# Kernel tuning notes

Hardware: AMD Instinct MI355X
Metric: run time of the kernel (lower is better)

The kernel has to match this reference:

```python
import jax, jax.numpy as jnp
import numpy as np

NEG_SLOPE = 0.2  # LeakyReLU(0.2)
DN = ('NCDHW', 'OIDHW', 'NCDHW')


def leaky(x):
    return jnp.where(x >= 0, x, NEG_SLOPE * x)


def conv3d(x, w, stride=1, pad=1):
    return jax.lax.conv_general_dilated(
        x, w, (stride,) * 3, [(pad, pad)] * 3, dimension_numbers=DN)


def down_mask(m):
    # active output sites of a k=3, s=2, p=1 sparse conv = maxpool of input mask
    return jax.lax.reduce_window(
        m, 0.0, jax.lax.max, (1, 1, 3, 3, 3), (1, 1, 2, 2, 2),
        [(0, 0), (0, 0), (1, 1), (1, 1), (1, 1)])


def res_block(x, m, wa, wb, wdn):
    # SubMConv3d == dense conv masked to active sites (inactive inputs are zero)
    identity = conv3d(x, wdn, 1, 0) * m if wdn is not None else x
    out = leaky(conv3d(x, wa) * m)
    out = conv3d(out, wb) * m
    return leaky(out + identity)


def setup_inputs() -> dict:
    key = jax.random.key(0)
    ks = jax.random.split(key, 12)
    B, D = 2, 64
    occ = jax.random.uniform(ks[0], (B, 1, D, D, D)) < 0.05
    mask = occ.astype(jnp.float32)
    x = jax.random.normal(ks[1], (B, 3, D, D, D), jnp.float32) * mask

    def w(k, o, i, ksz):
        fan = i * ksz ** 3
        return jax.random.normal(k, (o, i, ksz, ksz, ksz), jnp.float32) / np.sqrt(fan).astype(np.float32)

    return {
        'x': x, 'mask': mask,
        # stage1 (in 3 -> 64), has 1x1 downsample
        'w1a': w(ks[2], 64, 3, 3), 'w1b': w(ks[3], 64, 64, 3), 'w1d': w(ks[4], 64, 3, 1),
        'wd1': w(ks[5], 128, 64, 3),   # down1 stride 2
        'w2a': w(ks[6], 128, 128, 3), 'w2b': w(ks[7], 128, 128, 3),  # stage2
        'wd2': w(ks[8], 256, 128, 3),  # down2 stride 2
        'w3a': w(ks[9], 256, 256, 3), 'w3b': w(ks[10], 256, 256, 3),  # stage3
        'wd3': w(ks[11], 128, 256, 3),  # down3 stride 2 -> out_ch=128
    }


def reference(x, mask, w1a, w1b, w1d, wd1, w2a, w2b, wd2, w3a, w3b, wd3):
    m1 = mask
    m2 = down_mask(m1)
    m3 = down_mask(m2)

    x1 = res_block(x, m1, w1a, w1b, w1d)          # [B,64,64,64,64]
    x = leaky(conv3d(x1, wd1, stride=2))           # [B,128,32,32,32]
    x2 = res_block(x, m2, w2a, w2b, None)
    x = leaky(conv3d(x2, wd2, stride=2))           # [B,256,16,16,16]
    x3 = res_block(x, m3, w3a, w3b, None)
    x4 = leaky(conv3d(x3, wd3, stride=2))          # [B,128,8,8,8] == x4.dense()

    avg = x4.mean(axis=(2, 3, 4))
    mx = x4.max(axis=(2, 3, 4))
    return jnp.concatenate([avg, mx], axis=1)      # [B,256]
```

## Files before the change

### kernel.cpp

```cpp
#include <hip/hip_runtime.h>


enum { EPI_MASK = 1, EPI_LEAKY = 2, EPI_RESID = 4 };
#define ROWCAP 32768

typedef short  bf16x8 __attribute__((ext_vector_type(8)));
typedef float  f32x4  __attribute__((ext_vector_type(4)));
typedef ushort us4    __attribute__((ext_vector_type(4)));

__device__ __forceinline__ float leaky(float v) { return v >= 0.f ? v : 0.2f * v; }
__device__ __forceinline__ ushort f2bf(float f) {
    unsigned u = __float_as_uint(f);
    return (ushort)((u + 0x7FFFu + ((u >> 16) & 1u)) >> 16);
}
__device__ __forceinline__ float bf2f(ushort h) {
    return __uint_as_float((unsigned)h << 16);
}
__device__ __forceinline__ int choff(int c) {
    return (c >> 5) * 64 + ((c >> 3) & 3) * 16 + (c & 7);
}

__global__ __launch_bounds__(256) void transpose_w_kernel(
    const float* __restrict__ w, float* __restrict__ wT, int CO, int CIK)
{
    int i = blockIdx.x * 256 + threadIdx.x;
    if (i >= CO * CIK) return;
    int co = i / CIK, r = i - co * CIK;
    wT[(size_t)r * CO + co] = w[i];
}

__global__ __launch_bounds__(256) void pack_w1b_kernel(
    const float* __restrict__ w, float* __restrict__ wT)
{
    int i = blockIdx.x * 256 + threadIdx.x;
    if (i >= 27 * 64 * 64) return;
    int co = i & 63, ci = (i >> 6) & 63, t = i >> 12;
    wT[i] = w[(co * 64 + ci) * 27 + t];
}

__global__ __launch_bounds__(256) void pack_w_kernel(
    const float* __restrict__ w, ushort* __restrict__ A, int CI, int CO)
{
    int i = blockIdx.x * 256 + threadIdx.x;
    if (i >= 27 * CI * CO * 2) return;
    int j = i & 7, hilo = (i >> 3) & 1, L = (i >> 4) & 63, rest = i >> 10;
    int NMT = CO >> 4, NCI = CI >> 5;
    int mt = rest % NMT; rest /= NMT;
    int ct = rest % NCI;
    int tap = rest / NCI;
    int co = mt * 16 + (L & 15);
    int ci = ct * 32 + (L >> 4) * 8 + j;
    float v = w[((size_t)co * CI + ci) * 27 + tap];
    ushort h = f2bf(v);
    A[i] = hilo ? f2bf(v - bf2f(h)) : h;
}

template<int DIN, int DOUT>
__global__ __launch_bounds__(256) void maxpool_kernel(
    const float* __restrict__ in, float* __restrict__ out)
{
    int i = blockIdx.x * 256 + threadIdx.x;
    constexpr int D3O = DOUT * DOUT * DOUT;
    if (i >= 2 * D3O) return;
    int b = i / D3O;
    int v = i - b * D3O;
    int z = v / (DOUT * DOUT), y = (v / DOUT) % DOUT, x = v % DOUT;
    float mx = 0.f;
    #pragma unroll
    for (int dz = 0; dz < 3; ++dz)
        #pragma unroll
        for (int dy = 0; dy < 3; ++dy)
            #pragma unroll
            for (int dx = 0; dx < 3; ++dx) {
                int zi = 2 * z - 1 + dz, yi = 2 * y - 1 + dy, xi = 2 * x - 1 + dx;
                if ((unsigned)zi < (unsigned)DIN && (unsigned)yi < (unsigned)DIN &&
                    (unsigned)xi < (unsigned)DIN)
                    mx = fmaxf(mx, in[(size_t)b * DIN * DIN * DIN + (zi * DIN + yi) * DIN + xi]);
            }
    out[i] = mx;
}

__global__ __launch_bounds__(256) void build_list_kernel(
    const float* __restrict__ m, int* __restrict__ list, int* __restrict__ idxmap,
    int* __restrict__ count)
{
    int i = blockIdx.x * 256 + threadIdx.x;
    if (i >= 2 * 262144) return;
    if (m[i] > 0.5f) {
        int k = atomicAdd(count, 1);
        if (k < ROWCAP) {
            list[k] = i;
            idxmap[i] = k;
        }
    }
}

__global__ __launch_bounds__(64) void stage1a_kernel(
    const float* __restrict__ x, const float* __restrict__ waT,
    const int* __restrict__ list, const int* __restrict__ count,
    float* __restrict__ t1c)
{
    __shared__ float smem[81];
    int n = min(*count, ROWCAP);
    for (int i = blockIdx.x; i < n; i += gridDim.x) {
        int lin = list[i];
        int b = lin >> 18;
        int v = lin & 262143;
        int z = v >> 12, y = (v >> 6) & 63, xx = v & 63;
        for (int j = threadIdx.x; j < 81; j += 64) {
            int ci = j / 27, t = j - ci * 27;
            int zz = z + t / 9 - 1, yy = y + (t / 3) % 3 - 1, xc = xx + t % 3 - 1;
            float val = 0.f;
            if ((unsigned)zz < 64u && (unsigned)yy < 64u && (unsigned)xc < 64u)
                val = x[(size_t)(b * 3 + ci) * 262144 + (zz << 12) + (yy << 6) + xc];
            smem[j] = val;
        }
        __syncthreads();
        float acc = 0.f;
        #pragma unroll 9
        for (int j = 0; j < 81; ++j)
            acc = fmaf(smem[j], waT[j * 64 + threadIdx.x], acc);
        t1c[(size_t)i * 64 + threadIdx.x] = leaky(acc);
        __syncthreads();
    }
}

__global__ __launch_bounds__(64) void stage1b_kernel(
    const float* __restrict__ t1c, const float* __restrict__ x,
    const float* __restrict__ w1bT,
    const float* __restrict__ wdT,
    const int* __restrict__ list, const int* __restrict__ idxmap,
    const int* __restrict__ count,
    float* __restrict__ x1c)
{
    __shared__ int   srr[27];
    __shared__ float sx[27][64];
    int n = min(*count, ROWCAP);
    int i = blockIdx.x;
    if (i >= n) return;
    const int tid = threadIdx.x;
    int lin = list[i];
    int b = lin >> 18;
    int v = lin & 262143;
    int z = v >> 12, y = (v >> 6) & 63, xx = v & 63;
    const int* im = idxmap + b * 262144;

    if (tid < 27) {
        int kz = tid / 9, ky = (tid / 3) % 3, kx = tid % 3;
        int zz = z + kz - 1, yy = y + ky - 1, xc = xx + kx - 1;
        int r = -1;
        if ((unsigned)zz < 64u && (unsigned)yy < 64u && (unsigned)xc < 64u)
            r = im[(zz << 12) + (yy << 6) + xc];
        srr[tid] = r;
    }
    __syncthreads();
    #pragma unroll 1
    for (int t = 0; t < 27; ++t) {
        int r = srr[t];
        if (r >= 0)
            sx[t][tid] = t1c[(size_t)r * 64 + tid];
    }
    __syncthreads();

    float acc = 0.f;
    #pragma unroll 1
    for (int t = 0; t < 27; ++t) {
        if (srr[t] < 0) continue;
        const float* wp = w1bT + (size_t)t * 4096 + tid;
        const float* xr = sx[t];
        #pragma unroll 8
        for (int ci = 0; ci < 64; ++ci)
            acc = fmaf(xr[ci], wp[ci * 64], acc);
    }
    float id = 0.f;
    #pragma unroll
    for (int ci = 0; ci < 3; ++ci)
        id = fmaf(x[(size_t)(b * 3 + ci) * 262144 + v], wdT[ci * 64 + tid], id);
    x1c[(size_t)i * 64 + tid] = leaky(acc + id);
}

__global__ __launch_bounds__(128) void wd1_kernel(
    const float* __restrict__ x1c, const int* __restrict__ idxmap,
    const float* __restrict__ wT,
    ushort* __restrict__ outp)
{
    __shared__ int   srr[27];
    __shared__ float sx[27][64];
    const int tid = threadIdx.x;
    const int v = blockIdx.x;
    const int b = blockIdx.y;
    const int zo = v >> 10, yo = (v >> 5) & 31, xo = v & 31;
    const int* im = idxmap + b * 262144;

    if (tid < 27) {
        int kz = tid / 9, ky = (tid / 3) % 3, kx = tid % 3;
        int zi = 2 * zo - 1 + kz, yi = 2 * yo - 1 + ky, xi = 2 * xo - 1 + kx;
        int r = -1;
        if ((unsigned)zi < 64u && (unsigned)yi < 64u && (unsigned)xi < 64u)
            r = im[(zi << 12) + (yi << 6) + xi];
        srr[tid] = r;
    }
    __syncthreads();
    #pragma unroll 1
    for (int t = 0; t < 27; ++t) {
        int r = srr[t];
        if (r >= 0 && tid < 64)
            sx[t][tid] = x1c[(size_t)r * 64 + tid];
    }
    __syncthreads();

    float acc = 0.f;
    #pragma unroll 1
    for (int t = 0; t < 27; ++t) {
        if (srr[t] < 0) continue;
        const float* wp = wT + (size_t)t * 128 + tid;
        const float* xr = sx[t];
        #pragma unroll 8
        for (int ci = 0; ci < 64; ++ci)
            acc = fmaf(xr[ci], wp[(size_t)ci * 27 * 128], acc);
    }
    float val = leaky(acc);
    ushort hb = f2bf(val);
    ushort lb = f2bf(val - bf2f(hb));
    size_t vb = ((((size_t)b * 32 + zo) * 32 + yo) * 33 + xo) * 256 + 256;
    int off = choff(tid);
    outp[vb + off] = hb;
    outp[vb + off + 8] = lb;
}

template<int CI, int CO, int DI, int DO, int STRIDE, int RY, int NX, int NCT, int WPEU, int EPI>
__global__ __launch_bounds__(256, WPEU) void mfma_conv6_kernel(
    const ushort* __restrict__ inp, const ushort* __restrict__ A,
    const float* __restrict__ mask, const ushort* __restrict__ resid,
    ushort* __restrict__ outp)
{
    constexpr int NCI = CI / 32;
    constexpr int NMT = CO / 16;
    constexpr int CV = CI * 2;
    constexpr int CVO = CO * 2;
    constexpr int YG = DO / RY;
    constexpr int NXV = (DO - 1) * STRIDE + 3;
    constexpr int LVS = (STRIDE == 2) ? 68 : 72;
    constexpr int NGRP = RY * NXV * 8;

    __shared__ ushort sB[RY * NXV * LVS];

    const int rg = (blockIdx.x & 7) * ((int)gridDim.x >> 3) + (blockIdx.x >> 3);
    const int y0 = (rg % YG) * RY;
    const int z = (rg / YG) % DO;
    const int b = rg / (YG * DO);
    const int wave = threadIdx.x >> 6;
    const int lane = threadIdx.x & 63;
    const int n_l = lane & 15;
    const int q = lane >> 4;
    const int mt0 = (blockIdx.y * 4 + wave) * NCT;

    f32x4 acc[NCT][RY][NX];
    #pragma unroll
    for (int a = 0; a < NCT; ++a)
        #pragma unroll
        for (int r = 0; r < RY; ++r)
            #pragma unroll
            for (int c = 0; c < NX; ++c)
                acc[a][r][c] = (f32x4){0.f, 0.f, 0.f, 0.f};

    #pragma unroll 1
    for (int ct = 0; ct < NCI; ++ct) {
        #pragma unroll 1
        for (int dz = 0; dz < 3; ++dz) {
            int zp = z * STRIDE + dz - 1;
            bool vz = (unsigned)zp < (unsigned)DI;
            int zpc = vz ? zp : 0;
            #pragma unroll 1
            for (int dy = 0; dy < 3; ++dy) {
                long rowb[RY];
                #pragma unroll
                for (int ry = 0; ry < RY; ++ry) {
                    int yp = (y0 + ry) * STRIDE + dy - 1;
                    bool v = vz && ((unsigned)yp < (unsigned)DI);
                    rowb[ry] = v ? (((((long)b * DI + zpc) * DI + yp) * (DI + 1)) * CV + CV) : -1;
                }
                __syncthreads();
                for (int g = threadIdx.x; g < NGRP; g += 256) {
                    int r = g / (NXV * 8);
                    int rem = g - r * (NXV * 8);
                    int xv = rem >> 3;
                    int gg = rem & 7;
                    long src = (rowb[r] >= 0)
                             ? (rowb[r] + (long)(xv - 1) * CV + ct * 64 + gg * 8)
                             : (long)(ct * 64 + gg * 8);
                    *(bf16x8*)(sB + (r * NXV + xv) * LVS + gg * 8) = *(const bf16x8*)(inp + src);
                }
                __syncthreads();
                #pragma unroll
                for (int dx = 0; dx < 3; ++dx) {
                    const int tap = dz * 9 + dy * 3 + dx;
                    bf16x8 bh[RY][NX], bl[RY][NX];
                    #pragma unroll
                    for (int ry = 0; ry < RY; ++ry)
                        #pragma unroll
                        for (int nx = 0; nx < NX; ++nx) {
                            int xv = (nx * 16 + n_l) * STRIDE + dx;
                            const ushort* p = sB + (ry * NXV + xv) * LVS + q * 16;
                            bh[ry][nx] = *(const bf16x8*)p;
                            bl[ry][nx] = *(const bf16x8*)(p + 8);
                        }
                    bf16x8 ahf[NCT], alf[NCT];
                    #pragma unroll
                    for (int mt = 0; mt < NCT; ++mt) {
                        size_t aa = ((size_t)(tap * NCI + ct) * NMT + (mt0 + mt)) * 1024 + lane * 16;
                        ahf[mt] = *(const bf16x8*)(A + aa);
                        alf[mt] = *(const bf16x8*)(A + aa + 8);
                    }
                    #pragma unroll
                    for (int mt = 0; mt < NCT; ++mt)
                        #pragma unroll
                        for (int ry = 0; ry < RY; ++ry)
                            #pragma unroll
                            for (int nx = 0; nx < NX; ++nx)
                                acc[mt][ry][nx] = __builtin_amdgcn_mfma_f32_16x16x32_bf16(ahf[mt], bh[ry][nx], acc[mt][ry][nx], 0, 0, 0);
                    #pragma unroll
                    for (int mt = 0; mt < NCT; ++mt)
                        #pragma unroll
                        for (int ry = 0; ry < RY; ++ry)
                            #pragma unroll
                            for (int nx = 0; nx < NX; ++nx)
                                acc[mt][ry][nx] = __builtin_amdgcn_mfma_f32_16x16x32_bf16(ahf[mt], bl[ry][nx], acc[mt][ry][nx], 0, 0, 0);
                    #pragma unroll
                    for (int mt = 0; mt < NCT; ++mt)
                        #pragma unroll
                        for (int ry = 0; ry < RY; ++ry)
                            #pragma unroll
                            for (int nx = 0; nx < NX; ++nx)
                                acc[mt][ry][nx] = __builtin_amdgcn_mfma_f32_16x16x32_bf16(alf[mt], bh[ry][nx], acc[mt][ry][nx], 0, 0, 0);
                }
            }
        }
    }

    #pragma unroll
    for (int ry = 0; ry < RY; ++ry) {
        int yo = y0 + ry;
        #pragma unroll
        for (int nx = 0; nx < NX; ++nx) {
            int xo = nx * 16 + n_l;
            size_t vb = ((((size_t)b * DO + z) * DO + yo) * (DO + 1)) * CVO + CVO + (size_t)xo * CVO;
            float mval = 1.f;
            if (EPI & EPI_MASK) mval = mask[(((size_t)b * DO + z) * DO + yo) * DO + xo];
            #pragma unroll
            for (int mt = 0; mt < NCT; ++mt) {
                int c0 = (mt0 + mt) * 16 + q * 4;
                size_t oa = vb + choff(c0);
                float rs[4] = {0.f, 0.f, 0.f, 0.f};
                if (EPI & EPI_RESID) {
                    us4 rh4 = *(const us4*)(resid + oa);
                    us4 rl4 = *(const us4*)(resid + oa + 8);
                    #pragma unroll
                    for (int r = 0; r < 4; ++r) rs[r] = bf2f(rh4[r]) + bf2f(rl4[r]);
                }
                us4 oh, ol;
                #pragma unroll
                for (int r = 0; r < 4; ++r) {
                    float v = acc[mt][ry][nx][r];
                    if (EPI & EPI_MASK) v *= mval;
                    if (EPI & EPI_RESID) v += rs[r];
                    if (EPI & EPI_LEAKY) v = leaky(v);
                    ushort hb = f2bf(v);
                    oh[r] = hb;
                    ol[r] = f2bf(v - bf2f(hb));
                }
                *(us4*)(outp + oa) = oh;
                *(us4*)(outp + oa + 8) = ol;
            }
        }
    }
}

template<int CI, int CO, int DI, int RY, int NCT, int KS, int WPEU>
__global__ __launch_bounds__(256, WPEU) void mfma_conv7_kernel(
    const ushort* __restrict__ inp, const ushort* __restrict__ A,
    float* __restrict__ part)
{
    constexpr int DO = DI;
    constexpr int NCI = CI / 32;
    constexpr int KCI = NCI / KS;
    constexpr int NMT = CO / 16;
    constexpr int CV = CI * 2;
    constexpr int YG = DO / RY;
    constexpr int NYR = RY + 2;
    constexpr int NXV = DO + 2;
    constexpr int LVS = 72;
    constexpr int NCOG = NMT / (4 * NCT);
    constexpr int D3 = DO * DO * DO;

    __shared__ ushort sB[3 * NYR * NXV * LVS];

    const int rg = (blockIdx.x & 7) * ((int)gridDim.x >> 3) + (blockIdx.x >> 3);
    const int y0 = (rg % YG) * RY;
    const int z = (rg / YG) % DO;
    const int b = rg / (YG * DO);
    const int wave = threadIdx.x >> 6;
    const int lane = threadIdx.x & 63;
    const int n_l = lane & 15;
    const int q = lane >> 4;
    const int cog = blockIdx.y % NCOG;
    const int kc = blockIdx.y / NCOG;
    const int mt0 = (cog * 4 + wave) * NCT;

    f32x4 acc[NCT][RY];
    #pragma unroll
    for (int a = 0; a < NCT; ++a)
        #pragma unroll
        for (int r = 0; r < RY; ++r)
            acc[a][r] = (f32x4){0.f, 0.f, 0.f, 0.f};

    #pragma unroll 1
    for (int ctl = 0; ctl < KCI; ++ctl) {
        const int ct = kc * KCI + ctl;
        __syncthreads();
        for (int g = threadIdx.x; g < 3 * NYR * NXV * 8; g += 256) {
            int row = g / (NXV * 8);
            int rem = g - row * (NXV * 8);
            int xv = rem >> 3;
            int gg = rem & 7;
            int zi = row / NYR, yr = row - zi * NYR;
            int zp = z + zi - 1;
            int yp = y0 + yr - 1;
            bool v = ((unsigned)zp < (unsigned)DI) & ((unsigned)yp < (unsigned)DI);
            long src = v ? ((((((long)b * DI + zp) * DI + yp) * (DI + 1)) * CV + CV)
                            + (long)(xv - 1) * CV + ct * 64 + gg * 8)
                         : (long)(ct * 64 + gg * 8);
            *(bf16x8*)(sB + (row * NXV + xv) * LVS + gg * 8) = *(const bf16x8*)(inp + src);
        }
        __syncthreads();
        #pragma unroll 1
        for (int dz = 0; dz < 3; ++dz) {
            #pragma unroll 1
            for (int dy = 0; dy < 3; ++dy) {
                #pragma unroll
                for (int dx = 0; dx < 3; ++dx) {
                    const int tap = dz * 9 + dy * 3 + dx;
                    bf16x8 bh[RY], bl[RY];
                    #pragma unroll
                    for (int ry = 0; ry < RY; ++ry) {
                        const ushort* p = sB + ((dz * NYR + ry + dy) * NXV + n_l + dx) * LVS + q * 16;
                        bh[ry] = *(const bf16x8*)p;
                        bl[ry] = *(const bf16x8*)(p + 8);
                    }
                    bf16x8 ahf[NCT], alf[NCT];
                    #pragma unroll
                    for (int mt = 0; mt < NCT; ++mt) {
                        size_t aa = ((size_t)(tap * NCI + ct) * NMT + (mt0 + mt)) * 1024 + lane * 16;
                        ahf[mt] = *(const bf16x8*)(A + aa);
                        alf[mt] = *(const bf16x8*)(A + aa + 8);
                    }
                    #pragma unroll
                    for (int mt = 0; mt < NCT; ++mt)
                        #pragma unroll
                        for (int ry = 0; ry < RY; ++ry)
                            acc[mt][ry] = __builtin_amdgcn_mfma_f32_16x16x32_bf16(ahf[mt], bh[ry], acc[mt][ry], 0, 0, 0);
                    #pragma unroll
                    for (int mt = 0; mt < NCT; ++mt)
                        #pragma unroll
                        for (int ry = 0; ry < RY; ++ry)
                            acc[mt][ry] = __builtin_amdgcn_mfma_f32_16x16x32_bf16(ahf[mt], bl[ry], acc[mt][ry], 0, 0, 0);
                    #pragma unroll
                    for (int mt = 0; mt < NCT; ++mt)
                        #pragma unroll
                        for (int ry = 0; ry < RY; ++ry)
                            acc[mt][ry] = __builtin_amdgcn_mfma_f32_16x16x32_bf16(alf[mt], bh[ry], acc[mt][ry], 0, 0, 0);
                }
            }
        }
    }

    #pragma unroll
    for (int ry = 0; ry < RY; ++ry) {
        int yo = y0 + ry;
        int v = (z * DO + yo) * DO + n_l;
        #pragma unroll
        for (int mt = 0; mt < NCT; ++mt) {
            int c0 = (mt0 + mt) * 16 + q * 4;
            size_t off = (((size_t)kc * 2 + b) * D3 + v) * CO + c0;
            *(f32x4*)(part + off) = acc[mt][ry];
        }
    }
}

__global__ __launch_bounds__(256) void combine3_kernel(
    const float* __restrict__ part, const float* __restrict__ mask,
    const ushort* __restrict__ resid, ushort* __restrict__ outp)
{
    int i = blockIdx.x * 256 + threadIdx.x;
    if (i >= 2 * 4096 * 64) return;
    int g = i & 63, v = (i >> 6) & 4095, b = i >> 18;
    int c0 = g * 4;
    size_t p0 = (((size_t)b) * 4096 + v) * 256 + c0;
    float4 s0 = *(const float4*)(part + p0);
    float4 s1 = *(const float4*)(part + p0 + (size_t)2 * 4096 * 256);
    float m = mask[b * 4096 + v];
    int z = v >> 8, y = (v >> 4) & 15, x = v & 15;
    size_t vb = ((((size_t)b * 16 + z) * 16 + y) * 17) * 512 + 512 + (size_t)x * 512;
    size_t oa = vb + choff(c0);
    float rs[4] = {0.f, 0.f, 0.f, 0.f};
    if (resid) {
        us4 rh = *(const us4*)(resid + oa);
        us4 rl = *(const us4*)(resid + oa + 8);
        #pragma unroll
        for (int r = 0; r < 4; ++r) rs[r] = bf2f(rh[r]) + bf2f(rl[r]);
    }
    float sv[4] = {s0.x + s1.x, s0.y + s1.y, s0.z + s1.z, s0.w + s1.w};
    us4 oh, ol;
    #pragma unroll
    for (int r = 0; r < 4; ++r) {
        float val = sv[r] * m + rs[r];
        val = leaky(val);
        ushort hb = f2bf(val);
        oh[r] = hb;
        ol[r] = f2bf(val - bf2f(hb));
    }
    *(us4*)(outp + oa) = oh;
    *(us4*)(outp + oa + 8) = ol;
}

__global__ __launch_bounds__(256) void wd3_mfma_kernel(
    const ushort* __restrict__ x3, const ushort* __restrict__ A,
    float* __restrict__ x4)
{
    constexpr int NCI = 8;
    constexpr int NMT = 8;
    const int blk = blockIdx.x;
    const int yg = blk & 3;
    const int z = (blk >> 2) & 7;
    const int b = blk >> 5;
    const int wave = threadIdx.x >> 6;
    const int lane = threadIdx.x & 63;
    const int n_l = lane & 15;
    const int q = lane >> 4;
    const int y = yg * 2 + (n_l >> 3);
    const int x = n_l & 7;
    const int mt0 = wave * 2;

    f32x4 acc[2];
    acc[0] = (f32x4){0.f, 0.f, 0.f, 0.f};
    acc[1] = (f32x4){0.f, 0.f, 0.f, 0.f};
    const bf16x8 zero8 = {0, 0, 0, 0, 0, 0, 0, 0};

    for (int ct = 0; ct < NCI; ++ct) {
        #pragma unroll
        for (int dz = 0; dz < 3; ++dz) {
            int zp = 2 * z + dz - 1;
            if ((unsigned)zp >= 16u) continue;
            #pragma unroll
            for (int dy = 0; dy < 3; ++dy) {
                int yp = 2 * y + dy - 1;
                bool vy = (unsigned)yp < 16u;
                int ypc = vy ? yp : 0;
                #pragma unroll
                for (int dx = 0; dx < 3; ++dx) {
                    int xp = 2 * x + dx - 1;
                    int tap = dz * 9 + dy * 3 + dx;
                    size_t ba = ((((size_t)b * 16 + zp) * 16 + ypc) * 17 + 1 + xp) * 512
                              + ct * 64 + q * 16;
                    bf16x8 bh = vy ? *(const bf16x8*)(x3 + ba) : zero8;
                    bf16x8 bl = vy ? *(const bf16x8*)(x3 + ba + 8) : zero8;
                    bf16x8 ahf[2], alf[2];
                    #pragma unroll
                    for (int mt = 0; mt < 2; ++mt) {
                        size_t aa = ((size_t)(tap * NCI + ct) * NMT + (mt0 + mt)) * 1024 + lane * 16;
                        ahf[mt] = *(const bf16x8*)(A + aa);
                        alf[mt] = *(const bf16x8*)(A + aa + 8);
                    }
                    #pragma unroll
                    for (int mt = 0; mt < 2; ++mt)
                        acc[mt] = __builtin_amdgcn_mfma_f32_16x16x32_bf16(ahf[mt], bh, acc[mt], 0, 0, 0);
                    #pragma unroll
                    for (int mt = 0; mt < 2; ++mt)
                        acc[mt] = __builtin_amdgcn_mfma_f32_16x16x32_bf16(ahf[mt], bl, acc[mt], 0, 0, 0);
                    #pragma unroll
                    for (int mt = 0; mt < 2; ++mt)
                        acc[mt] = __builtin_amdgcn_mfma_f32_16x16x32_bf16(alf[mt], bh, acc[mt], 0, 0, 0);
                }
            }
        }
    }
    #pragma unroll
    for (int mt = 0; mt < 2; ++mt)
        #pragma unroll
        for (int r = 0; r < 4; ++r) {
            int co = (mt0 + mt) * 16 + q * 4 + r;
            x4[((size_t)(b * 128 + co)) * 512 + z * 64 + y * 8 + x] = leaky(acc[mt][r]);
        }
}

__global__ __launch_bounds__(64) void reduce_kernel(
    const float* __restrict__ x4, float* __restrict__ out)
{
    int bc = blockIdx.x;
    int b = bc >> 7, c = bc & 127;
    const float* p = x4 + (size_t)(b * 128 + c) * 512;
    float s = 0.f, mx = -3.4e38f;
    for (int i = threadIdx.x; i < 512; i += 64) {
        float v = p[i];
        s += v;
        mx = fmaxf(mx, v);
    }
    #pragma unroll
    for (int o = 32; o > 0; o >>= 1) {
        s += __shfl_down(s, o);
        mx = fmaxf(mx, __shfl_down(mx, o));
    }
    if (threadIdx.x == 0) {
        out[b * 256 + c] = s * (1.f / 512.f);
        out[b * 256 + 128 + c] = mx;
    }
}

__global__ __launch_bounds__(256) void zero_out_kernel(float* __restrict__ out, int n)
{
    int i = blockIdx.x * 256 + threadIdx.x;
    if (i < n) out[i] = 0.f;
}

extern "C" void kernel_launch(void* const* d_in, const int* in_sizes, int n_in,
                              void* d_out, int out_size, void* d_ws, size_t ws_size,
                              hipStream_t stream)
{
    (void)in_sizes; (void)n_in;
    const float* x    = (const float*)d_in[0];
    const float* mask = (const float*)d_in[1];
    const float* w1a  = (const float*)d_in[2];
    const float* w1b  = (const float*)d_in[3];
    const float* w1d  = (const float*)d_in[4];
    const float* wd1  = (const float*)d_in[5];
    const float* w2a  = (const float*)d_in[6];
    const float* w2b  = (const float*)d_in[7];
    const float* wd2  = (const float*)d_in[8];
    const float* w3a  = (const float*)d_in[9];
    const float* w3b  = (const float*)d_in[10];
    const float* wd3  = (const float*)d_in[11];
    float* out = (float*)d_out;
    char* ws = (char*)d_ws;

    const size_t RSZ = 34603520;
    const size_t SZ3 = 8913920;
    const size_t POFF = 9437184;
    char* R1 = ws;
    char* R2 = ws + RSZ;
    char* R3 = ws + 2 * RSZ;
    size_t off = 3 * RSZ;
    auto alloc = [&](size_t bytes) { char* p = ws + off; off = (off + bytes + 255) & ~255ull; return p; };
    ushort* pk2a = (ushort*)alloc(1769472);
    ushort* pk2b = (ushort*)alloc(1769472);
    ushort* pkd2 = (ushort*)alloc(3538944);
    ushort* pk3a = (ushort*)alloc(7077888);
    ushort* pk3b = (ushort*)alloc(7077888);
    float*  wd1T = (float*)alloc(884736);
    float*  waT  = (float*)alloc(20736);
    float*  w1bT = (float*)alloc(442368);
    float*  wdTt = (float*)alloc(768);
    float*  m2   = (float*)alloc(262144);
    float*  m3   = (float*)alloc(32768);
    int*    cnt  = (int*)alloc(256);
    const size_t NEED = off;

    if (ws_size < NEED) {
        zero_out_kernel<<<dim3((out_size + 255) / 256), 256, 0, stream>>>(out, out_size);
        return;
    }

    float* t1c  = (float*)R2;
    float* x1c  = (float*)(R2 + 8388608);
    int*   idx  = (int*)(R2 + 16777216);
    int*   list = (int*)(R2 + 18874368);
    ushort* pkd3 = (ushort*)R1;
    float*  x4   = (float*)R2;
    float*  part3a = (float*)(R2 + POFF);
    float*  part3b = (float*)(R3 + POFF);

    ushort* xin2 = (ushort*)R1;
    ushort* t2   = (ushort*)R2;
    ushort* x2   = (ushort*)R3;
    ushort* xin3 = (ushort*)R1;
    ushort* t3   = (ushort*)R2;
    ushort* x3   = (ushort*)R3;

    hipMemsetAsync(cnt, 0, 4, stream);
    hipMemsetAsync(idx, 0xFF, 2097152, stream);
    hipMemsetAsync(R1, 0, RSZ, stream);

    auto tg = [](int n) { return dim3((n + 255) / 256); };
    pack_w_kernel<<<tg(27 * 128 * 128 * 2), 256, 0, stream>>>(w2a, pk2a, 128, 128);
    pack_w_kernel<<<tg(27 * 128 * 128 * 2), 256, 0, stream>>>(w2b, pk2b, 128, 128);
    pack_w_kernel<<<tg(27 * 128 * 256 * 2), 256, 0, stream>>>(wd2, pkd2, 128, 256);
    pack_w_kernel<<<tg(27 * 256 * 256 * 2), 256, 0, stream>>>(w3a, pk3a, 256, 256);
    pack_w_kernel<<<tg(27 * 256 * 256 * 2), 256, 0, stream>>>(w3b, pk3b, 256, 256);
    transpose_w_kernel <<<tg(128 * 1728), 256, 0, stream>>>(wd1, wd1T, 128, 1728);
    transpose_w_kernel <<<tg(64 * 81),    256, 0, stream>>>(w1a, waT,  64, 81);
    pack_w1b_kernel    <<<tg(27 * 64 * 64), 256, 0, stream>>>(w1b, w1bT);
    transpose_w_kernel <<<tg(64 * 3),     256, 0, stream>>>(w1d, wdTt, 64, 3);

    maxpool_kernel<64, 32><<<dim3(2 * 32768 / 256), 256, 0, stream>>>(mask, m2);
    maxpool_kernel<32, 16><<<dim3(2 * 4096 / 256),  256, 0, stream>>>(m2, m3);
    build_list_kernel<<<dim3(2 * 262144 / 256), 256, 0, stream>>>(mask, list, idx, cnt);

    stage1a_kernel<<<dim3(2048), 64, 0, stream>>>(x, waT, list, cnt, t1c);
    stage1b_kernel<<<dim3(ROWCAP), 64, 0, stream>>>(t1c, x, w1bT, wdTt, list, idx, cnt, x1c);
    wd1_kernel<<<dim3(32768, 2), 128, 0, stream>>>(x1c, idx, wd1T, xin2);

    hipMemsetAsync(R2, 0, RSZ, stream);
    hipMemsetAsync(R3, 0, RSZ, stream);

    mfma_conv6_kernel<128, 128, 32, 32, 1, 2, 2, 2, 4, EPI_MASK | EPI_LEAKY>
        <<<dim3(1024, 1), 256, 0, stream>>>(xin2, pk2a, m2, nullptr, t2);
    mfma_conv6_kernel<128, 128, 32, 32, 1, 2, 2, 2, 4, EPI_MASK | EPI_RESID | EPI_LEAKY>
        <<<dim3(1024, 1), 256, 0, stream>>>(t2, pk2b, m2, xin2, x2);

    hipMemsetAsync(R1, 0, SZ3, stream);
    mfma_conv6_kernel<128, 256, 32, 16, 2, 2, 1, 2, 4, EPI_LEAKY>
        <<<dim3(256, 2), 256, 0, stream>>>(x2, pkd2, nullptr, nullptr, xin3);

    hipMemsetAsync(R2, 0, SZ3, stream);
    mfma_conv7_kernel<256, 256, 16, 2, 2, 2, 4>
        <<<dim3(256, 4), 256, 0, stream>>>(xin3, pk3a, part3a);
    combine3_kernel<<<dim3(2048), 256, 0, stream>>>(part3a, m3, nullptr, t3);

    hipMemsetAsync(R3, 0, SZ3, stream);
    mfma_conv7_kernel<256, 256, 16, 2, 2, 2, 4>
        <<<dim3(256, 4), 256, 0, stream>>>(t3, pk3b, part3b);
    combine3_kernel<<<dim3(2048), 256, 0, stream>>>(part3b, m3, xin3, x3);

    pack_w_kernel<<<tg(27 * 256 * 128 * 2), 256, 0, stream>>>(wd3, pkd3, 256, 128);
    wd3_mfma_kernel<<<dim3(64), 256, 0, stream>>>(x3, pkd3, x4);

    reduce_kernel<<<dim3(256), 64, 0, stream>>>(x4, out);
}
```

Before: 1.207 ms.

## Stage y-halo slab in shared memory once per dz for stage-2 convs

Adds a new conv kernel for the stride-1 stage-2 convolutions. For each (channel tile, dz) it loads a slab of RY+2 input rows with halo into shared memory, then loops over all dy and dx taps from that slab. The old kernel appears to reload per dy row. This cuts global-to-LDS traffic and barrier count by reusing the y halo, at the cost of a larger shared buffer, which may lower occupancy.

```diff
diff --git a/kernel.cpp b/kernel.cpp
--- a/kernel.cpp
+++ b/kernel.cpp
@@ -302,6 +302,151 @@
                         for (int nx = 0; nx < NX; ++nx) {
                             int xv = (nx * 16 + n_l) * STRIDE + dx;
                             const ushort* p = sB + (ry * NXV + xv) * LVS + q * 16;
+                            bh[ry][nx] = *(const bf16x8*)p;
+                            bl[ry][nx] = *(const bf16x8*)(p + 8);
+                        }
+                    bf16x8 ahf[NCT], alf[NCT];
+                    #pragma unroll
+                    for (int mt = 0; mt < NCT; ++mt) {
+                        size_t aa = ((size_t)(tap * NCI + ct) * NMT + (mt0 + mt)) * 1024 + lane * 16;
+                        ahf[mt] = *(const bf16x8*)(A + aa);
+                        alf[mt] = *(const bf16x8*)(A + aa + 8);
+                    }
+                    #pragma unroll
+                    for (int mt = 0; mt < NCT; ++mt)
+                        #pragma unroll
+                        for (int ry = 0; ry < RY; ++ry)
+                            #pragma unroll
+                            for (int nx = 0; nx < NX; ++nx)
+                                acc[mt][ry][nx] = __builtin_amdgcn_mfma_f32_16x16x32_bf16(ahf[mt], bh[ry][nx], acc[mt][ry][nx], 0, 0, 0);
+                    #pragma unroll
+                    for (int mt = 0; mt < NCT; ++mt)
+                        #pragma unroll
+                        for (int ry = 0; ry < RY; ++ry)
+                            #pragma unroll
+                            for (int nx = 0; nx < NX; ++nx)
+                                acc[mt][ry][nx] = __builtin_amdgcn_mfma_f32_16x16x32_bf16(ahf[mt], bl[ry][nx], acc[mt][ry][nx], 0, 0, 0);
+                    #pragma unroll
+                    for (int mt = 0; mt < NCT; ++mt)
+                        #pragma unroll
+                        for (int ry = 0; ry < RY; ++ry)
+                            #pragma unroll
+                            for (int nx = 0; nx < NX; ++nx)
+                                acc[mt][ry][nx] = __builtin_amdgcn_mfma_f32_16x16x32_bf16(alf[mt], bh[ry][nx], acc[mt][ry][nx], 0, 0, 0);
+                }
+            }
+        }
+    }
+
+    #pragma unroll
+    for (int ry = 0; ry < RY; ++ry) {
+        int yo = y0 + ry;
+        #pragma unroll
+        for (int nx = 0; nx < NX; ++nx) {
+            int xo = nx * 16 + n_l;
+            size_t vb = ((((size_t)b * DO + z) * DO + yo) * (DO + 1)) * CVO + CVO + (size_t)xo * CVO;
+            float mval = 1.f;
+            if (EPI & EPI_MASK) mval = mask[(((size_t)b * DO + z) * DO + yo) * DO + xo];
+            #pragma unroll
+            for (int mt = 0; mt < NCT; ++mt) {
+                int c0 = (mt0 + mt) * 16 + q * 4;
+                size_t oa = vb + choff(c0);
+                float rs[4] = {0.f, 0.f, 0.f, 0.f};
+                if (EPI & EPI_RESID) {
+                    us4 rh4 = *(const us4*)(resid + oa);
+                    us4 rl4 = *(const us4*)(resid + oa + 8);
+                    #pragma unroll
+                    for (int r = 0; r < 4; ++r) rs[r] = bf2f(rh4[r]) + bf2f(rl4[r]);
+                }
+                us4 oh, ol;
+                #pragma unroll
+                for (int r = 0; r < 4; ++r) {
+                    float v = acc[mt][ry][nx][r];
+                    if (EPI & EPI_MASK) v *= mval;
+                    if (EPI & EPI_RESID) v += rs[r];
+                    if (EPI & EPI_LEAKY) v = leaky(v);
+                    ushort hb = f2bf(v);
+                    oh[r] = hb;
+                    ol[r] = f2bf(v - bf2f(hb));
+                }
+                *(us4*)(outp + oa) = oh;
+                *(us4*)(outp + oa + 8) = ol;
+            }
+        }
+    }
+}
+
+template<int CI, int CO, int DI, int RY, int NX, int NCT, int WPEU, int EPI>
+__global__ __launch_bounds__(256, WPEU) void mfma_conv8_kernel(
+    const ushort* __restrict__ inp, const ushort* __restrict__ A,
+    const float* __restrict__ mask, const ushort* __restrict__ resid,
+    ushort* __restrict__ outp)
+{
+    constexpr int DO = DI;
+    constexpr int NCI = CI / 32;
+    constexpr int NMT = CO / 16;
+    constexpr int CV = CI * 2;
+    constexpr int CVO = CO * 2;
+    constexpr int YG = DO / RY;
+    constexpr int NYR = RY + 2;
+    constexpr int NXV = DO + 2;
+    constexpr int LVS = 72;
+    constexpr int NGRP = NYR * NXV * 8;
+
+    __shared__ ushort sB[NYR * NXV * LVS];
+
+    const int rg = (blockIdx.x & 7) * ((int)gridDim.x >> 3) + (blockIdx.x >> 3);
+    const int y0 = (rg % YG) * RY;
+    const int z = (rg / YG) % DO;
+    const int b = rg / (YG * DO);
+    const int wave = threadIdx.x >> 6;
+    const int lane = threadIdx.x & 63;
+    const int n_l = lane & 15;
+    const int q = lane >> 4;
+    const int mt0 = (blockIdx.y * 4 + wave) * NCT;
+
+    f32x4 acc[NCT][RY][NX];
+    #pragma unroll
+    for (int a = 0; a < NCT; ++a)
+        #pragma unroll
+        for (int r = 0; r < RY; ++r)
+            #pragma unroll
+            for (int c = 0; c < NX; ++c)
+                acc[a][r][c] = (f32x4){0.f, 0.f, 0.f, 0.f};
+
+    #pragma unroll 1
+    for (int ct = 0; ct < NCI; ++ct) {
+        #pragma unroll 1
+        for (int dz = 0; dz < 3; ++dz) {
+            int zp = z + dz - 1;
+            bool vz = (unsigned)zp < (unsigned)DI;
+            int zpc = vz ? zp : 0;
+            __syncthreads();
+            for (int g = threadIdx.x; g < NGRP; g += 256) {
+                int r = g / (NXV * 8);
+                int rem = g - r * (NXV * 8);
+                int xv = rem >> 3;
+                int gg = rem & 7;
+                int yp = y0 + r - 1;
+                bool v = vz & ((unsigned)yp < (unsigned)DI);
+                long src = v ? ((((((long)b * DI + zpc) * DI + yp) * (DI + 1)) * CV + CV)
+                                + (long)(xv - 1) * CV + ct * 64 + gg * 8)
+                             : (long)(ct * 64 + gg * 8);
+                *(bf16x8*)(sB + (r * NXV + xv) * LVS + gg * 8) = *(const bf16x8*)(inp + src);
+            }
+            __syncthreads();
+            #pragma unroll 1
+            for (int dy = 0; dy < 3; ++dy) {
+                #pragma unroll
+                for (int dx = 0; dx < 3; ++dx) {
+                    const int tap = dz * 9 + dy * 3 + dx;
+                    bf16x8 bh[RY][NX], bl[RY][NX];
+                    #pragma unroll
+                    for (int ry = 0; ry < RY; ++ry)
+                        #pragma unroll
+                        for (int nx = 0; nx < NX; ++nx) {
+                            int xv = nx * 16 + n_l + dx;
+                            const ushort* p = sB + ((ry + dy) * NXV + xv) * LVS + q * 16;
                             bh[ry][nx] = *(const bf16x8*)p;
                             bl[ry][nx] = *(const bf16x8*)(p + 8);
                         }
@@ -711,9 +856,9 @@
     hipMemsetAsync(R2, 0, RSZ, stream);
     hipMemsetAsync(R3, 0, RSZ, stream);
 
-    mfma_conv6_kernel<128, 128, 32, 32, 1, 2, 2, 2, 4, EPI_MASK | EPI_LEAKY>
+    mfma_conv8_kernel<128, 128, 32, 2, 2, 2, 4, EPI_MASK | EPI_LEAKY>
         <<<dim3(1024, 1), 256, 0, stream>>>(xin2, pk2a, m2, nullptr, t2);
-    mfma_conv6_kernel<128, 128, 32, 32, 1, 2, 2, 2, 4, EPI_MASK | EPI_RESID | EPI_LEAKY>
+    mfma_conv8_kernel<128, 128, 32, 2, 2, 2, 4, EPI_MASK | EPI_RESID | EPI_LEAKY>
         <<<dim3(1024, 1), 256, 0, stream>>>(t2, pk2b, m2, xin2, x2);
 
     hipMemsetAsync(R1, 0, SZ3, stream);
```

Result: faster. 1.123 ms (-7.0%).
